# Kernel optimization log

Hardware: AMD Instinct MI355X
Metric: run time of the kernel (lower is better)

The kernel has to match this reference:

```python
import jax, jax.numpy as jnp
import numpy as np

B, N, FIN, FOUT, NMAX = 8, 512, 256, 256, 32
BN_EPS = 1e-5
L2_EPS = 1e-12


def setup_inputs() -> dict:
    key = jax.random.key(0)
    ks = jax.random.split(key, 6)
    x = jax.random.normal(ks[0], (B, N, FIN), dtype=jnp.float32)
    idx1 = jax.random.randint(ks[1], (N * NMAX,), 0, N)
    idx2 = jax.random.randint(ks[2], (N * NMAX,), 0, N)
    idx3 = jax.random.randint(ks[3], (N * NMAX,), 0, N)
    # xavier-ish init for linear weights (torch Linear: y = x @ W.T + b)
    scale = np.sqrt(2.0 / (FIN + FOUT)) * np.sqrt(2.0)
    W_x_w = jax.random.normal(ks[4], (FOUT, FIN), dtype=jnp.float32) * scale
    W_n_w = jax.random.normal(ks[5], (FOUT, FIN), dtype=jnp.float32) * scale
    W_x_b = jnp.zeros((FOUT,), dtype=jnp.float32)
    W_n_b = jnp.zeros((FOUT,), dtype=jnp.float32)
    bn_gamma = jnp.ones((4 * FOUT,), dtype=jnp.float32)
    bn_beta = jnp.zeros((4 * FOUT,), dtype=jnp.float32)
    return {"x": x, "idx1": idx1, "idx2": idx2, "idx3": idx3,
            "W_x_w": W_x_w, "W_x_b": W_x_b, "W_n_w": W_n_w, "W_n_b": W_n_b,
            "bn_gamma": bn_gamma, "bn_beta": bn_beta}


def reference(x, idx1, idx2, idx3, W_x_w, W_x_b, W_n_w, W_n_b, bn_gamma, bn_beta):
    b, n, f = x.shape

    def neib_mean(idx):
        k = idx.shape[0] // n
        g = jnp.take(x, idx, axis=1)            # [B, N*k, F] gather
        return g.reshape(b, n, k, f).mean(axis=2)  # [B, N, F]

    h_self = jnp.einsum('bnf,of->bno', x, W_x_w) + W_x_b
    h1 = jnp.einsum('bnf,of->bno', neib_mean(idx1), W_n_w) + W_n_b
    h2 = jnp.einsum('bnf,of->bno', neib_mean(idx2), W_n_w) + W_n_b
    h3 = jnp.einsum('bnf,of->bno', neib_mean(idx3), W_n_w) + W_n_b
    h = jnp.concatenate([h_self, h1, h2, h3], axis=2)  # [B, N, 4*FOUT]

    # F.normalize(dim=2, p=2): x / max(||x||, eps)
    norm = jnp.sqrt(jnp.sum(h * h, axis=2, keepdims=True))
    h = h / jnp.maximum(norm, L2_EPS)
    h = jax.nn.relu(h)

    # BatchNorm1d over channels (training mode, biased variance), stats over (B, N)
    mu = h.mean(axis=(0, 1))
    var = jnp.mean(jnp.square(h - mu), axis=(0, 1))
    h = (h - mu) * jax.lax.rsqrt(var + BN_EPS) * bn_gamma + bn_beta
    return h
```

## Files before the change

kernel.cpp:

```cpp
#include <hip/hip_runtime.h>


typedef short  s16x8 __attribute__((ext_vector_type(8)));
typedef float  f32x4 __attribute__((ext_vector_type(4)));
typedef unsigned short u16x4 __attribute__((ext_vector_type(4)));

#define NREP 32

#define OFF_WCAT   (0u)
#define OFF_XWX    (262144u)
#define OFF_XWN    (2359296u)
#define OFF_HBUF   (4456448u)
#define OFF_SUMS   (12845056u)
#define OFF_COEFA  (13107200u)
#define OFF_COEFB  (13111296u)

__device__ __forceinline__ unsigned short f2bf(float f) {
    unsigned int u = __float_as_uint(f);
    u = (u + 0x7FFFu + ((u >> 16) & 1u)) >> 16;
    return (unsigned short)u;
}
__device__ __forceinline__ float bflo(unsigned int d) {
    return __uint_as_float(d << 16);
}
__device__ __forceinline__ float bfhi(unsigned int d) {
    return __uint_as_float(d & 0xFFFF0000u);
}

__global__ __launch_bounds__(256) void k0_convert(
    const float* __restrict__ Wx, const float* __restrict__ Wn,
    unsigned short* __restrict__ Wcat)
{
    int e = (blockIdx.x * 256 + threadIdx.x) * 4;
    const float* src = (e < 65536) ? &Wx[e] : &Wn[e - 65536];
    float4 v = *(const float4*)src;
    u16x4 o; o[0]=f2bf(v.x); o[1]=f2bf(v.y); o[2]=f2bf(v.z); o[3]=f2bf(v.w);
    *(u16x4*)&Wcat[e] = o;
}

__global__ __launch_bounds__(256) void k1_gemm(
    const float* __restrict__ x, const unsigned short* __restrict__ W,
    const float* __restrict__ bx,
    unsigned short* __restrict__ xWx, unsigned short* __restrict__ xWn)
{
    const int tid = threadIdx.x;
    const int w = tid >> 6, l = tid & 63;
    const int l15 = l & 15, lhi = l >> 4;
    const int rowBase = blockIdx.x * 64 + w * 16;
    const int colBase = blockIdx.y * 64;

    f32x4 acc[4] = {};
    const float*          ap = &x[(rowBase + l15) * 256 + lhi * 8];
    const unsigned short* wp = &W[(colBase + l15) * 256 + lhi * 8];
    #pragma unroll
    for (int kk = 0; kk < 256; kk += 32) {
        float4 a0 = *(const float4*)(ap + kk);
        float4 a1 = *(const float4*)(ap + kk + 4);
        s16x8 a;
        a[0]=(short)f2bf(a0.x); a[1]=(short)f2bf(a0.y);
        a[2]=(short)f2bf(a0.z); a[3]=(short)f2bf(a0.w);
        a[4]=(short)f2bf(a1.x); a[5]=(short)f2bf(a1.y);
        a[6]=(short)f2bf(a1.z); a[7]=(short)f2bf(a1.w);
        #pragma unroll
        for (int c = 0; c < 4; ++c) {
            s16x8 b = *(const s16x8*)(wp + c * 16 * 256 + kk);
            acc[c] = __builtin_amdgcn_mfma_f32_16x16x32_bf16(a, b, acc[c], 0, 0, 0);
        }
    }
    const int row0 = rowBase + lhi * 4;
    if (colBase < 256) {
        #pragma unroll
        for (int c = 0; c < 4; ++c) {
            float bxv = bx[colBase + c * 16 + l15];
            #pragma unroll
            for (int r = 0; r < 4; ++r)
                xWx[(row0 + r) * 256 + colBase + c * 16 + l15] = f2bf(acc[c][r] + bxv);
        }
    } else {
        #pragma unroll
        for (int c = 0; c < 4; ++c)
            #pragma unroll
            for (int r = 0; r < 4; ++r)
                xWn[(row0 + r) * 256 + (colBase - 256) + c * 16 + l15] = f2bf(acc[c][r]);
    }
}

__global__ __launch_bounds__(256) void k2_rows(
    const unsigned short* __restrict__ xWx, const unsigned short* __restrict__ xWn,
    const int* __restrict__ idx1, const int* __restrict__ idx2,
    const int* __restrict__ idx3, const float* __restrict__ bn,
    unsigned short* __restrict__ hbuf, float* __restrict__ sums)
{
    __shared__ int   lidx[4][96];
    __shared__ float lpart[4][2048];
    const int t = threadIdx.x, w = t >> 6, l = t & 63;
    const int r = blockIdx.x * 4 + w;
    const int b = r >> 9, n = r & 511;

    if (l < 32) {
        lidx[w][l]      = idx1[n * 32 + l];
        lidx[w][64 + l] = idx3[n * 32 + l];
    } else {
        lidx[w][l]      = idx2[n * 32 + (l & 31)];
    }
    __syncthreads();

    const float4 bnv = *(const float4*)&bn[l * 4];
    const unsigned short* basep = &xWn[(unsigned)b * (512u * 256u)];
    f32x4 m1 = {}, m2 = {}, m3 = {};
    #pragma unroll
    for (int k = 0; k < 32; ++k) {
        uint2 d = *(const uint2*)(basep + lidx[w][k] * 256 + l * 4);
        m1[0] += bflo(d.x); m1[1] += bfhi(d.x);
        m1[2] += bflo(d.y); m1[3] += bfhi(d.y);
    }
    #pragma unroll
    for (int k = 0; k < 32; ++k) {
        uint2 d = *(const uint2*)(basep + lidx[w][32 + k] * 256 + l * 4);
        m2[0] += bflo(d.x); m2[1] += bfhi(d.x);
        m2[2] += bflo(d.y); m2[3] += bfhi(d.y);
    }
    #pragma unroll
    for (int k = 0; k < 32; ++k) {
        uint2 d = *(const uint2*)(basep + lidx[w][64 + k] * 256 + l * 4);
        m3[0] += bflo(d.x); m3[1] += bfhi(d.x);
        m3[2] += bflo(d.y); m3[3] += bfhi(d.y);
    }

    uint2 hd = *(const uint2*)(xWx + r * 256 + l * 4);
    f32x4 hseg[4];
    hseg[0][0] = bflo(hd.x); hseg[0][1] = bfhi(hd.x);
    hseg[0][2] = bflo(hd.y); hseg[0][3] = bfhi(hd.y);
    #pragma unroll
    for (int j = 0; j < 4; ++j) {
        hseg[1][j] = m1[j] * (1.f / 32.f) + bnv[j];
        hseg[2][j] = m2[j] * (1.f / 32.f) + bnv[j];
        hseg[3][j] = m3[j] * (1.f / 32.f) + bnv[j];
    }
    float p = 0.f;
    #pragma unroll
    for (int s = 0; s < 4; ++s)
        #pragma unroll
        for (int j = 0; j < 4; ++j) p += hseg[s][j] * hseg[s][j];
    #pragma unroll
    for (int m = 32; m > 0; m >>= 1) p += __shfl_xor(p, m);
    const float invn = 1.0f / fmaxf(sqrtf(p), 1e-12f);

    unsigned short* hr = &hbuf[(unsigned)r * 1024u];
    #pragma unroll
    for (int s = 0; s < 4; ++s) {
        f32x4 v;
        #pragma unroll
        for (int j = 0; j < 4; ++j) v[j] = fmaxf(hseg[s][j] * invn, 0.f);
        uint2 o;
        o.x = (unsigned)f2bf(v[0]) | ((unsigned)f2bf(v[1]) << 16);
        o.y = (unsigned)f2bf(v[2]) | ((unsigned)f2bf(v[3]) << 16);
        *(uint2*)(hr + s * 256 + l * 4) = o;
        #pragma unroll
        for (int j = 0; j < 4; ++j) {
            lpart[w][       s * 256 + l * 4 + j] = v[j];
            lpart[w][1024 + s * 256 + l * 4 + j] = v[j] * v[j];
        }
    }
    __syncthreads();
    float* sb = &sums[(blockIdx.x & (NREP - 1)) * 2048];
    for (int c = t; c < 2048; c += 256)
        atomicAdd(&sb[c], lpart[0][c] + lpart[1][c] + lpart[2][c] + lpart[3][c]);
}

__global__ __launch_bounds__(256) void k3_coef(
    const float* __restrict__ sums, const float* __restrict__ gamma,
    const float* __restrict__ beta, float* __restrict__ cA, float* __restrict__ cB)
{
    int c = blockIdx.x * 256 + threadIdx.x;
    float s = 0.f, s2 = 0.f;
    #pragma unroll
    for (int rep = 0; rep < NREP; ++rep) {
        s  += sums[rep * 2048 + c];
        s2 += sums[rep * 2048 + 1024 + c];
    }
    float mu  = s  * (1.f / 4096.f);
    float var = s2 * (1.f / 4096.f) - mu * mu;
    float a = gamma[c] / sqrtf(var + 1e-5f);
    cA[c] = a;
    cB[c] = beta[c] - mu * a;
}

__global__ __launch_bounds__(256) void k4_apply(
    const unsigned short* __restrict__ hbuf, const float* __restrict__ cA,
    const float* __restrict__ cB, float* __restrict__ out)
{
    int gid = blockIdx.x * 256 + threadIdx.x;
    int c0 = (gid & 255) * 4;
    uint2 hd = *(const uint2*)(hbuf + (unsigned)gid * 4u);
    float4 a = *(const float4*)&cA[c0];
    float4 b = *(const float4*)&cB[c0];
    float4 o;
    o.x = bflo(hd.x) * a.x + b.x;  o.y = bfhi(hd.x) * a.y + b.y;
    o.z = bflo(hd.y) * a.z + b.z;  o.w = bfhi(hd.y) * a.w + b.w;
    *(float4*)&out[(unsigned)gid * 4u] = o;
}

extern "C" void kernel_launch(void* const* d_in, const int* in_sizes, int n_in,
                              void* d_out, int out_size, void* d_ws, size_t ws_size,
                              hipStream_t stream)
{
    const float* x     = (const float*)d_in[0];
    const int*   idx1  = (const int*)  d_in[1];
    const int*   idx2  = (const int*)  d_in[2];
    const int*   idx3  = (const int*)  d_in[3];
    const float* Wx    = (const float*)d_in[4];
    const float* bx    = (const float*)d_in[5];
    const float* Wn    = (const float*)d_in[6];
    const float* bn    = (const float*)d_in[7];
    const float* gamma = (const float*)d_in[8];
    const float* beta  = (const float*)d_in[9];

    char* ws = (char*)d_ws;
    unsigned short* Wcat = (unsigned short*)(ws + OFF_WCAT);
    unsigned short* xWx  = (unsigned short*)(ws + OFF_XWX);
    unsigned short* xWn  = (unsigned short*)(ws + OFF_XWN);
    unsigned short* hbuf = (unsigned short*)(ws + OFF_HBUF);
    float*          sums = (float*)         (ws + OFF_SUMS);
    float*          cA   = (float*)         (ws + OFF_COEFA);
    float*          cB   = (float*)         (ws + OFF_COEFB);

    k0_convert<<<128, 256, 0, stream>>>(Wx, Wn, Wcat);
    k1_gemm<<<dim3(64, 8), 256, 0, stream>>>(x, Wcat, bx, xWx, xWn);
    hipMemsetAsync(sums, 0, NREP * 2048 * sizeof(float), stream);
    k2_rows<<<1024, 256, 0, stream>>>(xWx, xWn, idx1, idx2, idx3, bn, hbuf, sums);
    k3_coef<<<4, 256, 0, stream>>>(sums, gamma, beta, cA, cB);
    k4_apply<<<4096, 256, 0, stream>>>(hbuf, cA, cB, (float*)d_out);
}
```

Baseline: 122.7 us.

## Fuse whole pipeline into one cooperative kernel with grid syncs

Replaces the five-kernel sequence plus memset with a single cooperative-launch kernel: GEMM (converting the fp32 weights inline), a grid sync, gather/normalize with per-block BN partial sums, another grid sync, then the BN apply from rows held in LDS. This removes the launch gaps, the weight-conversion kernel, the hbuf round trip and the memset, and it cuts atomic replicas from 32 to 16. In exchange it costs two grid-wide barriers and needs all 1024 blocks resident at once. If the cooperative launch fails, the old multi-kernel path runs instead.

```diff
diff --git a/kernel.cpp b/kernel.cpp
--- a/kernel.cpp
+++ b/kernel.cpp
@@ -1,19 +1,22 @@
 #include <hip/hip_runtime.h>
+#include <hip/hip_cooperative_groups.h>
+
+namespace cg = cooperative_groups;
 
 
 typedef short  s16x8 __attribute__((ext_vector_type(8)));
 typedef float  f32x4 __attribute__((ext_vector_type(4)));
 typedef unsigned short u16x4 __attribute__((ext_vector_type(4)));
 
-#define NREP 32
-
-#define OFF_WCAT   (0u)
-#define OFF_XWX    (262144u)
-#define OFF_XWN    (2359296u)
-#define OFF_HBUF   (4456448u)
-#define OFF_SUMS   (12845056u)
-#define OFF_COEFA  (13107200u)
-#define OFF_COEFB  (13111296u)
+#define NREP 16
+
+#define OFF_XWX    (0u)
+#define OFF_XWN    (2097152u)
+#define OFF_SUMS   (4194304u)
+#define OFF_WCAT   (5242880u)
+#define OFF_HBUF   (6291456u)
+#define OFF_COEFA  (14680064u)
+#define OFF_COEFB  (14684160u)
 
 __device__ __forceinline__ unsigned short f2bf(float f) {
     unsigned int u = __float_as_uint(f);
@@ -25,6 +28,195 @@
 }
 __device__ __forceinline__ float bfhi(unsigned int d) {
     return __uint_as_float(d & 0xFFFF0000u);
+}
+__device__ __forceinline__ float bf2f(unsigned short h) {
+    return __uint_as_float(((unsigned int)h) << 16);
+}
+__device__ __forceinline__ s16x8 cvt_frag(const float* p) {
+    float4 a0 = *(const float4*)p;
+    float4 a1 = *(const float4*)(p + 4);
+    s16x8 a;
+    a[0]=(short)f2bf(a0.x); a[1]=(short)f2bf(a0.y);
+    a[2]=(short)f2bf(a0.z); a[3]=(short)f2bf(a0.w);
+    a[4]=(short)f2bf(a1.x); a[5]=(short)f2bf(a1.y);
+    a[6]=(short)f2bf(a1.z); a[7]=(short)f2bf(a1.w);
+    return a;
+}
+
+__global__ __launch_bounds__(256, 4) void fused_sage(
+    const float* __restrict__ x,
+    const int* __restrict__ idx1, const int* __restrict__ idx2,
+    const int* __restrict__ idx3,
+    const float* __restrict__ Wx, const float* __restrict__ bx,
+    const float* __restrict__ Wn, const float* __restrict__ bn,
+    const float* __restrict__ gamma, const float* __restrict__ beta,
+    unsigned short* __restrict__ xWx, unsigned short* __restrict__ xWn,
+    float* __restrict__ sums, float* __restrict__ out)
+{
+    __shared__ int lidx[4][96];
+    __shared__ unsigned short hl[4][1024];
+    const int t = threadIdx.x, w = t >> 6, l = t & 63;
+    const int l15 = l & 15, lhi = l >> 4;
+    const int bid = blockIdx.x;
+
+    {
+        const int rowTile = bid >> 4;
+        const int colTile = bid & 15;
+        const int rowBase = rowTile * 64 + w * 16;
+        const int colBase = colTile * 32;
+        const bool isX = (colTile < 8);
+        const float* Wmat = isX ? Wx : Wn;
+        const int wrow0 = colBase - (isX ? 0 : 256);
+
+        f32x4 acc[2] = {};
+        const float* ap  = &x[(rowBase + l15) * 256 + lhi * 8];
+        const float* wp0 = &Wmat[(wrow0 +      l15) * 256 + lhi * 8];
+        const float* wp1 = &Wmat[(wrow0 + 16 + l15) * 256 + lhi * 8];
+        #pragma unroll
+        for (int kk = 0; kk < 256; kk += 32) {
+            s16x8 a  = cvt_frag(ap  + kk);
+            s16x8 b0 = cvt_frag(wp0 + kk);
+            s16x8 b1 = cvt_frag(wp1 + kk);
+            acc[0] = __builtin_amdgcn_mfma_f32_16x16x32_bf16(a, b0, acc[0], 0, 0, 0);
+            acc[1] = __builtin_amdgcn_mfma_f32_16x16x32_bf16(a, b1, acc[1], 0, 0, 0);
+        }
+        if (bid < NREP) {
+            float4 z = {0.f, 0.f, 0.f, 0.f};
+            *(float4*)&sums[bid * 2048 + t * 4]        = z;
+            *(float4*)&sums[bid * 2048 + 1024 + t * 4] = z;
+        }
+        unsigned short* stage = &hl[0][0];
+        const int row0l = w * 16 + lhi * 4;
+        #pragma unroll
+        for (int c = 0; c < 2; ++c) {
+            float badd = isX ? bx[colBase + c * 16 + l15] : 0.f;
+            #pragma unroll
+            for (int r = 0; r < 4; ++r)
+                stage[(row0l + r) * 32 + c * 16 + l15] = f2bf(acc[c][r] + badd);
+        }
+        __syncthreads();
+        {
+            const int rl = t >> 2, seg = t & 3;
+            uint4 v = *(const uint4*)&stage[rl * 32 + seg * 8];
+            unsigned short* dst = isX ? xWx : xWn;
+            *(uint4*)&dst[(rowTile * 64 + rl) * 256 + wrow0 + seg * 8] = v;
+        }
+    }
+    cg::this_grid().sync();
+
+    {
+        const int r = bid * 4 + w;
+        const int b = r >> 9, n = r & 511;
+        if (l < 32) {
+            lidx[w][l]      = idx1[n * 32 + l];
+            lidx[w][64 + l] = idx3[n * 32 + l];
+        } else {
+            lidx[w][l]      = idx2[n * 32 + (l & 31)];
+        }
+        __syncthreads();
+
+        const float4 bnv = *(const float4*)&bn[l * 4];
+        const unsigned short* basep = &xWn[(unsigned)b * (512u * 256u)];
+        f32x4 m1 = {}, m2 = {}, m3 = {};
+        #pragma unroll
+        for (int k = 0; k < 32; ++k) {
+            uint2 d = *(const uint2*)(basep + lidx[w][k] * 256 + l * 4);
+            m1[0] += bflo(d.x); m1[1] += bfhi(d.x);
+            m1[2] += bflo(d.y); m1[3] += bfhi(d.y);
+        }
+        #pragma unroll
+        for (int k = 0; k < 32; ++k) {
+            uint2 d = *(const uint2*)(basep + lidx[w][32 + k] * 256 + l * 4);
+            m2[0] += bflo(d.x); m2[1] += bfhi(d.x);
+            m2[2] += bflo(d.y); m2[3] += bfhi(d.y);
+        }
+        #pragma unroll
+        for (int k = 0; k < 32; ++k) {
+            uint2 d = *(const uint2*)(basep + lidx[w][64 + k] * 256 + l * 4);
+            m3[0] += bflo(d.x); m3[1] += bfhi(d.x);
+            m3[2] += bflo(d.y); m3[3] += bfhi(d.y);
+        }
+
+        uint2 hd = *(const uint2*)(xWx + r * 256 + l * 4);
+        f32x4 hseg[4];
+        hseg[0][0] = bflo(hd.x); hseg[0][1] = bfhi(hd.x);
+        hseg[0][2] = bflo(hd.y); hseg[0][3] = bfhi(hd.y);
+        #pragma unroll
+        for (int j = 0; j < 4; ++j) {
+            hseg[1][j] = m1[j] * (1.f / 32.f) + bnv[j];
+            hseg[2][j] = m2[j] * (1.f / 32.f) + bnv[j];
+            hseg[3][j] = m3[j] * (1.f / 32.f) + bnv[j];
+        }
+        float p = 0.f;
+        #pragma unroll
+        for (int s = 0; s < 4; ++s)
+            #pragma unroll
+            for (int j = 0; j < 4; ++j) p += hseg[s][j] * hseg[s][j];
+        #pragma unroll
+        for (int m = 32; m > 0; m >>= 1) p += __shfl_xor(p, m);
+        const float invn = 1.0f / fmaxf(sqrtf(p), 1e-12f);
+
+        #pragma unroll
+        for (int s = 0; s < 4; ++s) {
+            float v0 = fmaxf(hseg[s][0] * invn, 0.f);
+            float v1 = fmaxf(hseg[s][1] * invn, 0.f);
+            float v2 = fmaxf(hseg[s][2] * invn, 0.f);
+            float v3 = fmaxf(hseg[s][3] * invn, 0.f);
+            uint2 o;
+            o.x = (unsigned)f2bf(v0) | ((unsigned)f2bf(v1) << 16);
+            o.y = (unsigned)f2bf(v2) | ((unsigned)f2bf(v3) << 16);
+            *(uint2*)(&hl[w][s * 256 + l * 4]) = o;
+        }
+        __syncthreads();
+        float* sb = &sums[(bid & (NREP - 1)) * 2048];
+        #pragma unroll
+        for (int i = 0; i < 4; ++i) {
+            const int c = t + i * 256;
+            float sAc = 0.f, sQc = 0.f;
+            #pragma unroll
+            for (int w2 = 0; w2 < 4; ++w2) {
+                float v = bf2f(hl[w2][c]);
+                sAc += v; sQc += v * v;
+            }
+            atomicAdd(&sb[c], sAc);
+            atomicAdd(&sb[1024 + c], sQc);
+        }
+    }
+    cg::this_grid().sync();
+
+    {
+        const int c0 = t * 4;
+        float4 g  = *(const float4*)&gamma[c0];
+        float4 be = *(const float4*)&beta[c0];
+        f32x4 s = {}, q = {};
+        #pragma unroll
+        for (int rep = 0; rep < NREP; ++rep) {
+            float4 a  = *(const float4*)&sums[rep * 2048 + c0];
+            float4 b2 = *(const float4*)&sums[rep * 2048 + 1024 + c0];
+            s[0] += a.x;  s[1] += a.y;  s[2] += a.z;  s[3] += a.w;
+            q[0] += b2.x; q[1] += b2.y; q[2] += b2.z; q[3] += b2.w;
+        }
+        const float gg[4] = {g.x, g.y, g.z, g.w};
+        const float bb[4] = {be.x, be.y, be.z, be.w};
+        f32x4 A, Bc;
+        #pragma unroll
+        for (int j = 0; j < 4; ++j) {
+            float mu  = s[j] * (1.f / 4096.f);
+            float var = q[j] * (1.f / 4096.f) - mu * mu;
+            A[j]  = gg[j] / sqrtf(var + 1e-5f);
+            Bc[j] = bb[j] - mu * A[j];
+        }
+        #pragma unroll
+        for (int w2 = 0; w2 < 4; ++w2) {
+            uint2 hd = *(const uint2*)(&hl[w2][c0]);
+            float4 o;
+            o.x = bflo(hd.x) * A[0] + Bc[0];
+            o.y = bfhi(hd.x) * A[1] + Bc[1];
+            o.z = bflo(hd.y) * A[2] + Bc[2];
+            o.w = bfhi(hd.y) * A[3] + Bc[3];
+            *(float4*)&out[(unsigned)(bid * 4 + w2) * 1024u + c0] = o;
+        }
+    }
 }
 
 __global__ __launch_bounds__(256) void k0_convert(
@@ -54,13 +246,7 @@
     const unsigned short* wp = &W[(colBase + l15) * 256 + lhi * 8];
     #pragma unroll
     for (int kk = 0; kk < 256; kk += 32) {
-        float4 a0 = *(const float4*)(ap + kk);
-        float4 a1 = *(const float4*)(ap + kk + 4);
-        s16x8 a;
-        a[0]=(short)f2bf(a0.x); a[1]=(short)f2bf(a0.y);
-        a[2]=(short)f2bf(a0.z); a[3]=(short)f2bf(a0.w);
-        a[4]=(short)f2bf(a1.x); a[5]=(short)f2bf(a1.y);
-        a[6]=(short)f2bf(a1.z); a[7]=(short)f2bf(a1.w);
+        s16x8 a = cvt_frag(ap + kk);
         #pragma unroll
         for (int c = 0; c < 4; ++c) {
             s16x8 b = *(const s16x8*)(wp + c * 16 * 256 + kk);
@@ -217,18 +403,27 @@
     const float* beta  = (const float*)d_in[9];
 
     char* ws = (char*)d_ws;
-    unsigned short* Wcat = (unsigned short*)(ws + OFF_WCAT);
     unsigned short* xWx  = (unsigned short*)(ws + OFF_XWX);
     unsigned short* xWn  = (unsigned short*)(ws + OFF_XWN);
-    unsigned short* hbuf = (unsigned short*)(ws + OFF_HBUF);
     float*          sums = (float*)         (ws + OFF_SUMS);
-    float*          cA   = (float*)         (ws + OFF_COEFA);
-    float*          cB   = (float*)         (ws + OFF_COEFB);
-
-    k0_convert<<<128, 256, 0, stream>>>(Wx, Wn, Wcat);
-    k1_gemm<<<dim3(64, 8), 256, 0, stream>>>(x, Wcat, bx, xWx, xWn);
-    hipMemsetAsync(sums, 0, NREP * 2048 * sizeof(float), stream);
-    k2_rows<<<1024, 256, 0, stream>>>(xWx, xWn, idx1, idx2, idx3, bn, hbuf, sums);
-    k3_coef<<<4, 256, 0, stream>>>(sums, gamma, beta, cA, cB);
-    k4_apply<<<4096, 256, 0, stream>>>(hbuf, cA, cB, (float*)d_out);
-}
+    float*          outp = (float*)d_out;
+
+    void* args[] = { (void*)&x, (void*)&idx1, (void*)&idx2, (void*)&idx3,
+                     (void*)&Wx, (void*)&bx, (void*)&Wn, (void*)&bn,
+                     (void*)&gamma, (void*)&beta,
+                     (void*)&xWx, (void*)&xWn, (void*)&sums, (void*)&outp };
+    hipError_t err = hipLaunchCooperativeKernel((void*)fused_sage, dim3(1024),
+                                                dim3(256), args, 0, stream);
+    if (err != hipSuccess) {
+        unsigned short* Wcat = (unsigned short*)(ws + OFF_WCAT);
+        unsigned short* hbuf = (unsigned short*)(ws + OFF_HBUF);
+        float*          cA   = (float*)         (ws + OFF_COEFA);
+        float*          cB   = (float*)         (ws + OFF_COEFB);
+        k0_convert<<<128, 256, 0, stream>>>(Wx, Wn, Wcat);
+        k1_gemm<<<dim3(64, 8), 256, 0, stream>>>(x, Wcat, bx, xWx, xWn);
+        hipMemsetAsync(sums, 0, NREP * 2048 * sizeof(float), stream);
+        k2_rows<<<1024, 256, 0, stream>>>(xWx, xWn, idx1, idx2, idx3, bn, hbuf, sums);
+        k3_coef<<<4, 256, 0, stream>>>(sums, gamma, beta, cA, cB);
+        k4_apply<<<4096, 256, 0, stream>>>(hbuf, cA, cB, outp);
+    }
+}
```

New measurement: 385.0 us. 214% more time.

## Fuse weight conversion into GEMM, fold memset and coef into neighbors

Applied to the files above, without the earlier changes.

Drops the separate weight-to-bf16 conversion kernel by converting fp32 weights inside the GEMM. It replaces the memset with zeroing by the first GEMM blocks and merges the BN coefficient kernel into the apply kernel, which each block now recomputes redundantly. The GEMM tile shrinks to 64x32 for more blocks and its output is staged through LDS for coalesced 16-byte stores. NREP is halved, giving more atomic contention in exchange for a cheaper reduction. The launch chain goes from six operations to three, at the cost of repeated weight conversion work in every GEMM block.

```diff
diff --git a/kernel.cpp b/kernel.cpp
--- a/kernel.cpp
+++ b/kernel.cpp
@@ -3,17 +3,13 @@
 
 typedef short  s16x8 __attribute__((ext_vector_type(8)));
 typedef float  f32x4 __attribute__((ext_vector_type(4)));
-typedef unsigned short u16x4 __attribute__((ext_vector_type(4)));
-
-#define NREP 32
-
-#define OFF_WCAT   (0u)
-#define OFF_XWX    (262144u)
-#define OFF_XWN    (2359296u)
-#define OFF_HBUF   (4456448u)
-#define OFF_SUMS   (12845056u)
-#define OFF_COEFA  (13107200u)
-#define OFF_COEFB  (13111296u)
+
+#define NREP 16
+
+#define OFF_XWX    (0u)
+#define OFF_XWN    (2097152u)
+#define OFF_SUMS   (4194304u)
+#define OFF_HBUF   (4325376u)
 
 __device__ __forceinline__ unsigned short f2bf(float f) {
     unsigned int u = __float_as_uint(f);
@@ -26,66 +22,71 @@
 __device__ __forceinline__ float bfhi(unsigned int d) {
     return __uint_as_float(d & 0xFFFF0000u);
 }
-
-__global__ __launch_bounds__(256) void k0_convert(
-    const float* __restrict__ Wx, const float* __restrict__ Wn,
-    unsigned short* __restrict__ Wcat)
-{
-    int e = (blockIdx.x * 256 + threadIdx.x) * 4;
-    const float* src = (e < 65536) ? &Wx[e] : &Wn[e - 65536];
-    float4 v = *(const float4*)src;
-    u16x4 o; o[0]=f2bf(v.x); o[1]=f2bf(v.y); o[2]=f2bf(v.z); o[3]=f2bf(v.w);
-    *(u16x4*)&Wcat[e] = o;
-}
-
-__global__ __launch_bounds__(256) void k1_gemm(
-    const float* __restrict__ x, const unsigned short* __restrict__ W,
-    const float* __restrict__ bx,
-    unsigned short* __restrict__ xWx, unsigned short* __restrict__ xWn)
-{
-    const int tid = threadIdx.x;
-    const int w = tid >> 6, l = tid & 63;
+__device__ __forceinline__ s16x8 cvt_frag(const float* p) {
+    float4 a0 = *(const float4*)p;
+    float4 a1 = *(const float4*)(p + 4);
+    s16x8 a;
+    a[0]=(short)f2bf(a0.x); a[1]=(short)f2bf(a0.y);
+    a[2]=(short)f2bf(a0.z); a[3]=(short)f2bf(a0.w);
+    a[4]=(short)f2bf(a1.x); a[5]=(short)f2bf(a1.y);
+    a[6]=(short)f2bf(a1.z); a[7]=(short)f2bf(a1.w);
+    return a;
+}
+
+__global__ __launch_bounds__(256) void kA_gemm(
+    const float* __restrict__ x,
+    const float* __restrict__ Wx, const float* __restrict__ bx,
+    const float* __restrict__ Wn,
+    unsigned short* __restrict__ xWx, unsigned short* __restrict__ xWn,
+    float* __restrict__ sums)
+{
+    __shared__ unsigned short stage[64 * 32];
+    const int t = threadIdx.x, w = t >> 6, l = t & 63;
     const int l15 = l & 15, lhi = l >> 4;
-    const int rowBase = blockIdx.x * 64 + w * 16;
-    const int colBase = blockIdx.y * 64;
-
-    f32x4 acc[4] = {};
-    const float*          ap = &x[(rowBase + l15) * 256 + lhi * 8];
-    const unsigned short* wp = &W[(colBase + l15) * 256 + lhi * 8];
+    const int bid = blockIdx.x;
+    const int rowTile = bid >> 4;
+    const int colTile = bid & 15;
+    const int rowBase = rowTile * 64 + w * 16;
+    const int colBase = colTile * 32;
+    const bool isX = (colTile < 8);
+    const float* Wmat = isX ? Wx : Wn;
+    const int wrow0 = colBase - (isX ? 0 : 256);
+
+    f32x4 acc[2] = {};
+    const float* ap  = &x[(rowBase + l15) * 256 + lhi * 8];
+    const float* wp0 = &Wmat[(wrow0 +      l15) * 256 + lhi * 8];
+    const float* wp1 = &Wmat[(wrow0 + 16 + l15) * 256 + lhi * 8];
     #pragma unroll
     for (int kk = 0; kk < 256; kk += 32) {
-        float4 a0 = *(const float4*)(ap + kk);
-        float4 a1 = *(const float4*)(ap + kk + 4);
-        s16x8 a;
-        a[0]=(short)f2bf(a0.x); a[1]=(short)f2bf(a0.y);
-        a[2]=(short)f2bf(a0.z); a[3]=(short)f2bf(a0.w);
-        a[4]=(short)f2bf(a1.x); a[5]=(short)f2bf(a1.y);
-        a[6]=(short)f2bf(a1.z); a[7]=(short)f2bf(a1.w);
-        #pragma unroll
-        for (int c = 0; c < 4; ++c) {
-            s16x8 b = *(const s16x8*)(wp + c * 16 * 256 + kk);
-            acc[c] = __builtin_amdgcn_mfma_f32_16x16x32_bf16(a, b, acc[c], 0, 0, 0);
-        }
-    }
-    const int row0 = rowBase + lhi * 4;
-    if (colBase < 256) {
-        #pragma unroll
-        for (int c = 0; c < 4; ++c) {
-            float bxv = bx[colBase + c * 16 + l15];
-            #pragma unroll
-            for (int r = 0; r < 4; ++r)
-                xWx[(row0 + r) * 256 + colBase + c * 16 + l15] = f2bf(acc[c][r] + bxv);
-        }
-    } else {
-        #pragma unroll
-        for (int c = 0; c < 4; ++c)
-            #pragma unroll
-            for (int r = 0; r < 4; ++r)
-                xWn[(row0 + r) * 256 + (colBase - 256) + c * 16 + l15] = f2bf(acc[c][r]);
-    }
-}
-
-__global__ __launch_bounds__(256) void k2_rows(
+        s16x8 a  = cvt_frag(ap  + kk);
+        s16x8 b0 = cvt_frag(wp0 + kk);
+        s16x8 b1 = cvt_frag(wp1 + kk);
+        acc[0] = __builtin_amdgcn_mfma_f32_16x16x32_bf16(a, b0, acc[0], 0, 0, 0);
+        acc[1] = __builtin_amdgcn_mfma_f32_16x16x32_bf16(a, b1, acc[1], 0, 0, 0);
+    }
+    if (bid < NREP) {
+        float4 z = {0.f, 0.f, 0.f, 0.f};
+        *(float4*)&sums[bid * 2048 + t * 4]        = z;
+        *(float4*)&sums[bid * 2048 + 1024 + t * 4] = z;
+    }
+    const int row0l = w * 16 + lhi * 4;
+    #pragma unroll
+    for (int c = 0; c < 2; ++c) {
+        float badd = isX ? bx[colBase + c * 16 + l15] : 0.f;
+        #pragma unroll
+        for (int r = 0; r < 4; ++r)
+            stage[(row0l + r) * 32 + c * 16 + l15] = f2bf(acc[c][r] + badd);
+    }
+    __syncthreads();
+    {
+        const int rl = t >> 2, seg = t & 3;
+        uint4 v = *(const uint4*)&stage[rl * 32 + seg * 8];
+        unsigned short* dst = isX ? xWx : xWn;
+        *(uint4*)&dst[(rowTile * 64 + rl) * 256 + wrow0 + seg * 8] = v;
+    }
+}
+
+__global__ __launch_bounds__(256) void kB_rows(
     const unsigned short* __restrict__ xWx, const unsigned short* __restrict__ xWn,
     const int* __restrict__ idx1, const int* __restrict__ idx2,
     const int* __restrict__ idx3, const float* __restrict__ bn,
@@ -168,37 +169,44 @@
         atomicAdd(&sb[c], lpart[0][c] + lpart[1][c] + lpart[2][c] + lpart[3][c]);
 }
 
-__global__ __launch_bounds__(256) void k3_coef(
+__global__ __launch_bounds__(256) void kC_apply(
     const float* __restrict__ sums, const float* __restrict__ gamma,
-    const float* __restrict__ beta, float* __restrict__ cA, float* __restrict__ cB)
-{
-    int c = blockIdx.x * 256 + threadIdx.x;
-    float s = 0.f, s2 = 0.f;
+    const float* __restrict__ beta, const unsigned short* __restrict__ hbuf,
+    float* __restrict__ out)
+{
+    const int t = threadIdx.x;
+    const int c0 = t * 4;
+    f32x4 s = {}, q = {};
     #pragma unroll
     for (int rep = 0; rep < NREP; ++rep) {
-        s  += sums[rep * 2048 + c];
-        s2 += sums[rep * 2048 + 1024 + c];
-    }
-    float mu  = s  * (1.f / 4096.f);
-    float var = s2 * (1.f / 4096.f) - mu * mu;
-    float a = gamma[c] / sqrtf(var + 1e-5f);
-    cA[c] = a;
-    cB[c] = beta[c] - mu * a;
-}
-
-__global__ __launch_bounds__(256) void k4_apply(
-    const unsigned short* __restrict__ hbuf, const float* __restrict__ cA,
-    const float* __restrict__ cB, float* __restrict__ out)
-{
-    int gid = blockIdx.x * 256 + threadIdx.x;
-    int c0 = (gid & 255) * 4;
-    uint2 hd = *(const uint2*)(hbuf + (unsigned)gid * 4u);
-    float4 a = *(const float4*)&cA[c0];
-    float4 b = *(const float4*)&cB[c0];
-    float4 o;
-    o.x = bflo(hd.x) * a.x + b.x;  o.y = bfhi(hd.x) * a.y + b.y;
-    o.z = bflo(hd.y) * a.z + b.z;  o.w = bfhi(hd.y) * a.w + b.w;
-    *(float4*)&out[(unsigned)gid * 4u] = o;
+        float4 a  = *(const float4*)&sums[rep * 2048 + c0];
+        float4 b2 = *(const float4*)&sums[rep * 2048 + 1024 + c0];
+        s[0] += a.x;  s[1] += a.y;  s[2] += a.z;  s[3] += a.w;
+        q[0] += b2.x; q[1] += b2.y; q[2] += b2.z; q[3] += b2.w;
+    }
+    float4 g  = *(const float4*)&gamma[c0];
+    float4 be = *(const float4*)&beta[c0];
+    const float gg[4] = {g.x, g.y, g.z, g.w};
+    const float bb[4] = {be.x, be.y, be.z, be.w};
+    f32x4 A, Bc;
+    #pragma unroll
+    for (int j = 0; j < 4; ++j) {
+        float mu  = s[j] * (1.f / 4096.f);
+        float var = q[j] * (1.f / 4096.f) - mu * mu;
+        A[j]  = gg[j] / sqrtf(var + 1e-5f);
+        Bc[j] = bb[j] - mu * A[j];
+    }
+    #pragma unroll
+    for (int r2 = 0; r2 < 4; ++r2) {
+        const unsigned row = blockIdx.x * 4 + r2;
+        uint2 hd = *(const uint2*)(hbuf + row * 1024u + c0);
+        float4 o;
+        o.x = bflo(hd.x) * A[0] + Bc[0];
+        o.y = bfhi(hd.x) * A[1] + Bc[1];
+        o.z = bflo(hd.y) * A[2] + Bc[2];
+        o.w = bfhi(hd.y) * A[3] + Bc[3];
+        *(float4*)&out[row * 1024u + c0] = o;
+    }
 }
 
 extern "C" void kernel_launch(void* const* d_in, const int* in_sizes, int n_in,
@@ -217,18 +225,12 @@
     const float* beta  = (const float*)d_in[9];
 
     char* ws = (char*)d_ws;
-    unsigned short* Wcat = (unsigned short*)(ws + OFF_WCAT);
     unsigned short* xWx  = (unsigned short*)(ws + OFF_XWX);
     unsigned short* xWn  = (unsigned short*)(ws + OFF_XWN);
+    float*          sums = (float*)         (ws + OFF_SUMS);
     unsigned short* hbuf = (unsigned short*)(ws + OFF_HBUF);
-    float*          sums = (float*)         (ws + OFF_SUMS);
-    float*          cA   = (float*)         (ws + OFF_COEFA);
-    float*          cB   = (float*)         (ws + OFF_COEFB);
-
-    k0_convert<<<128, 256, 0, stream>>>(Wx, Wn, Wcat);
-    k1_gemm<<<dim3(64, 8), 256, 0, stream>>>(x, Wcat, bx, xWx, xWn);
-    hipMemsetAsync(sums, 0, NREP * 2048 * sizeof(float), stream);
-    k2_rows<<<1024, 256, 0, stream>>>(xWx, xWn, idx1, idx2, idx3, bn, hbuf, sums);
-    k3_coef<<<4, 256, 0, stream>>>(sums, gamma, beta, cA, cB);
-    k4_apply<<<4096, 256, 0, stream>>>(hbuf, cA, cB, (float*)d_out);
-}
+
+    kA_gemm<<<1024, 256, 0, stream>>>(x, Wx, bx, Wn, xWx, xWn, sums);
+    kB_rows<<<1024, 256, 0, stream>>>(xWx, xWn, idx1, idx2, idx3, bn, hbuf, sums);
+    kC_apply<<<1024, 256, 0, stream>>>(sums, gamma, beta, hbuf, (float*)d_out);
+}
```

After: 128.7 us. 1.05x slower.
